# Optimization experiments

Measured on AMD Instinct MI355X. Metric: run time of the kernel, lower is better.

Reference implementation:

```python
import jax, jax.numpy as jnp
import numpy as np


def _extract_patches_same(x, k):
    # x: [B, h, w, C] -> patches [B, h, w, C, k*k] (channel-major, patch-minor,
    # matching the depthwise-conv based extract_patches_xla layout that the
    # reshape (group, C//group, k^2) in CarafeConvolution assumes).
    b, h, w, c = x.shape
    pad = k // 2
    xp = jnp.pad(x, ((0, 0), (pad, pad), (pad, pad), (0, 0)))
    shifts = [xp[:, di:di + h, dj:dj + w, :] for di in range(k) for dj in range(k)]
    return jnp.stack(shifts, axis=-1)  # [B, h, w, C, k^2]


def _nearest_idx(out_size, in_size):
    # tf.image.resize nearest with half-pixel centers
    scale = in_size / out_size
    idx = jnp.floor((jnp.arange(out_size) + 0.5) * scale).astype(jnp.int32)
    return jnp.clip(idx, 0, in_size - 1)


def setup_inputs() -> dict:
    key = jax.random.key(0)
    k1, k2 = jax.random.split(key)
    features = jax.random.normal(k1, (2, 64, 64, 256), dtype=jnp.float32)
    masks = jax.random.uniform(k2, (2, 128, 128, 25), dtype=jnp.float32)
    return {"features": features, "masks": masks, "kernel_size": 5}


def reference(features, masks, kernel_size):
    k = kernel_size
    B, H, W, C1 = masks.shape
    _, h, w, C0 = features.shape
    group = C1 // (k * k)
    # im2col patch extraction at low resolution
    patches = _extract_patches_same(features, k)  # [B, h, w, C0, k^2]
    # nearest-neighbor upsample patches to mask resolution
    ih = _nearest_idx(H, h)
    iw = _nearest_idx(W, w)
    patches = patches[:, ih][:, :, iw]  # [B, H, W, C0, k^2]
    # grouped adaptive-kernel reassembly
    feats = patches.reshape(B, H, W, group, C0 // group, k * k)
    m = masks.reshape(B, H, W, group, k * k)
    out = jnp.einsum('bhwgcp,bhwgp->bhwgc', feats, m)
    return out.reshape(B, H, W, C0)
```

## Files before the change

kernel.cpp:

```cpp
#include <hip/hip_runtime.h>


#define C0   256
#define HLO  64
#define WLO  64
#define HHI  128
#define WHI  128
#define K    5
#define KK   25

__global__ __launch_bounds__(256) void carafe_quad_kernel(
    const float* __restrict__ feat,
    const float* __restrict__ mask,
    float* __restrict__ out)
{
    const int wid = __builtin_amdgcn_readfirstlane(
        blockIdx.x * 4 + (threadIdx.x >> 6));
    const int lane = threadIdx.x & 63;
    const int c    = lane * 4;

    const int b  = wid >> 12;
    const int y0 = (wid >> 6) & 63;
    const int x0 = wid & 63;

    const int Y0 = y0 * 2;
    const int X0 = x0 * 2;

    const float* fbase = feat + ((size_t)b * HLO * WLO) * C0;
    const float* mbase = mask + ((size_t)((b * HHI + Y0) * WHI + X0)) * KK;
    const float* m00 = mbase;
    const float* m01 = mbase + KK;
    const float* m10 = mbase + WHI * KK;
    const float* m11 = mbase + WHI * KK + KK;

    float4 a00 = make_float4(0.f, 0.f, 0.f, 0.f);
    float4 a01 = make_float4(0.f, 0.f, 0.f, 0.f);
    float4 a10 = make_float4(0.f, 0.f, 0.f, 0.f);
    float4 a11 = make_float4(0.f, 0.f, 0.f, 0.f);

    #pragma unroll
    for (int di = 0; di < K; ++di) {
        const int   y  = y0 + di - 2;
        const int   yc = min(max(y, 0), HLO - 1);
        const float vy = ((unsigned)y < (unsigned)HLO) ? 1.f : 0.f;
        #pragma unroll
        for (int dj = 0; dj < K; ++dj) {
            const int   x  = x0 + dj - 2;
            const int   xc = min(max(x, 0), WLO - 1);
            const float v  = ((unsigned)x < (unsigned)WLO) ? vy : 0.f;

            float4 f = *(const float4*)(fbase + (size_t)(yc * WLO + xc) * C0 + c);
            f.x *= v; f.y *= v; f.z *= v; f.w *= v;

            const int p = di * K + dj;
            const float w00 = m00[p];
            const float w01 = m01[p];
            const float w10 = m10[p];
            const float w11 = m11[p];
            a00.x = fmaf(f.x, w00, a00.x); a00.y = fmaf(f.y, w00, a00.y);
            a00.z = fmaf(f.z, w00, a00.z); a00.w = fmaf(f.w, w00, a00.w);
            a01.x = fmaf(f.x, w01, a01.x); a01.y = fmaf(f.y, w01, a01.y);
            a01.z = fmaf(f.z, w01, a01.z); a01.w = fmaf(f.w, w01, a01.w);
            a10.x = fmaf(f.x, w10, a10.x); a10.y = fmaf(f.y, w10, a10.y);
            a10.z = fmaf(f.z, w10, a10.z); a10.w = fmaf(f.w, w10, a10.w);
            a11.x = fmaf(f.x, w11, a11.x); a11.y = fmaf(f.y, w11, a11.y);
            a11.z = fmaf(f.z, w11, a11.z); a11.w = fmaf(f.w, w11, a11.w);
        }
    }

    float* obase = out + ((size_t)((b * HHI + Y0) * WHI + X0)) * C0 + c;
    *(float4*)(obase)                 = a00;
    *(float4*)(obase + C0)            = a01;
    *(float4*)(obase + WHI * C0)      = a10;
    *(float4*)(obase + WHI * C0 + C0) = a11;
}

extern "C" void kernel_launch(void* const* d_in, const int* in_sizes, int n_in,
                              void* d_out, int out_size, void* d_ws, size_t ws_size,
                              hipStream_t stream) {
    const float* feat = (const float*)d_in[0];
    const float* mask = (const float*)d_in[1];
    float* out = (float*)d_out;

    carafe_quad_kernel<<<8192 / 4, 256, 0, stream>>>(feat, mask, out);
}
```

Measured before the change: 79.89 us.

## Process two adjacent low-res columns per wave and remap blocks per XCD

Each wave now computes a 2x4 block of high-res outputs from two neighbouring low-res pixels. It walks a shared 6-wide window of feature columns, so one load feeds both pixels' 5x5 taps: 30 feature loads per row set instead of 50. Block indices are also remapped so that each XCD handles a contiguous range of (batch, row) pairs, which is meant to improve L2 locality of the feature reads. The cost is twice as many accumulators per thread and half as many waves, which lowers occupancy and latency hiding.

```diff
diff --git a/kernel.cpp b/kernel.cpp
--- a/kernel.cpp
+++ b/kernel.cpp
@@ -9,34 +9,36 @@
 #define K    5
 #define KK   25
 
-__global__ __launch_bounds__(256) void carafe_quad_kernel(
+__global__ __launch_bounds__(256) void carafe_kernel(
     const float* __restrict__ feat,
     const float* __restrict__ mask,
     float* __restrict__ out)
 {
-    const int wid = __builtin_amdgcn_readfirstlane(
-        blockIdx.x * 4 + (threadIdx.x >> 6));
+    const int wv   = __builtin_amdgcn_readfirstlane(threadIdx.x >> 6);
+    const int bid  = blockIdx.x;
+    const int xcd  = bid & 7;
+    const int i    = bid >> 3;
+    const int r    = xcd * 16 + (i & 15);
+    const int xblk = i >> 4;
+    const int b    = r >> 6;
+    const int y0   = r & 63;
+    const int x0   = xblk * 8 + wv * 2;
     const int lane = threadIdx.x & 63;
     const int c    = lane * 4;
-
-    const int b  = wid >> 12;
-    const int y0 = (wid >> 6) & 63;
-    const int x0 = wid & 63;
 
     const int Y0 = y0 * 2;
     const int X0 = x0 * 2;
 
-    const float* fbase = feat + ((size_t)b * HLO * WLO) * C0;
-    const float* mbase = mask + ((size_t)((b * HHI + Y0) * WHI + X0)) * KK;
-    const float* m00 = mbase;
-    const float* m01 = mbase + KK;
-    const float* m10 = mbase + WHI * KK;
-    const float* m11 = mbase + WHI * KK + KK;
+    const float* fbase = feat + (size_t)b * HLO * WLO * C0;
+    const float* mrow0 = mask + (size_t)((b * HHI + Y0) * WHI + X0) * KK;
+    const float* mrow1 = mrow0 + WHI * KK;
 
-    float4 a00 = make_float4(0.f, 0.f, 0.f, 0.f);
-    float4 a01 = make_float4(0.f, 0.f, 0.f, 0.f);
-    float4 a10 = make_float4(0.f, 0.f, 0.f, 0.f);
-    float4 a11 = make_float4(0.f, 0.f, 0.f, 0.f);
+    float4 acc[2][4];
+    #pragma unroll
+    for (int rr = 0; rr < 2; ++rr)
+        #pragma unroll
+        for (int qq = 0; qq < 4; ++qq)
+            acc[rr][qq] = make_float4(0.f, 0.f, 0.f, 0.f);
 
     #pragma unroll
     for (int di = 0; di < K; ++di) {
@@ -44,35 +46,53 @@
         const int   yc = min(max(y, 0), HLO - 1);
         const float vy = ((unsigned)y < (unsigned)HLO) ? 1.f : 0.f;
         #pragma unroll
-        for (int dj = 0; dj < K; ++dj) {
-            const int   x  = x0 + dj - 2;
+        for (int t = 0; t < 6; ++t) {
+            const int   x  = x0 + t - 2;
             const int   xc = min(max(x, 0), WLO - 1);
             const float v  = ((unsigned)x < (unsigned)WLO) ? vy : 0.f;
 
             float4 f = *(const float4*)(fbase + (size_t)(yc * WLO + xc) * C0 + c);
             f.x *= v; f.y *= v; f.z *= v; f.w *= v;
 
-            const int p = di * K + dj;
-            const float w00 = m00[p];
-            const float w01 = m01[p];
-            const float w10 = m10[p];
-            const float w11 = m11[p];
-            a00.x = fmaf(f.x, w00, a00.x); a00.y = fmaf(f.y, w00, a00.y);
-            a00.z = fmaf(f.z, w00, a00.z); a00.w = fmaf(f.w, w00, a00.w);
-            a01.x = fmaf(f.x, w01, a01.x); a01.y = fmaf(f.y, w01, a01.y);
-            a01.z = fmaf(f.z, w01, a01.z); a01.w = fmaf(f.w, w01, a01.w);
-            a10.x = fmaf(f.x, w10, a10.x); a10.y = fmaf(f.y, w10, a10.y);
-            a10.z = fmaf(f.z, w10, a10.z); a10.w = fmaf(f.w, w10, a10.w);
-            a11.x = fmaf(f.x, w11, a11.x); a11.y = fmaf(f.y, w11, a11.y);
-            a11.z = fmaf(f.z, w11, a11.z); a11.w = fmaf(f.w, w11, a11.w);
+            if (t <= 4) {
+                const int p = di * K + t;
+                #pragma unroll
+                for (int rr = 0; rr < 2; ++rr) {
+                    const float* mr = rr ? mrow1 : mrow0;
+                    #pragma unroll
+                    for (int qq = 0; qq < 2; ++qq) {
+                        const float wgt = mr[qq * KK + p];
+                        acc[rr][qq].x = fmaf(f.x, wgt, acc[rr][qq].x);
+                        acc[rr][qq].y = fmaf(f.y, wgt, acc[rr][qq].y);
+                        acc[rr][qq].z = fmaf(f.z, wgt, acc[rr][qq].z);
+                        acc[rr][qq].w = fmaf(f.w, wgt, acc[rr][qq].w);
+                    }
+                }
+            }
+            if (t >= 1) {
+                const int p = di * K + t - 1;
+                #pragma unroll
+                for (int rr = 0; rr < 2; ++rr) {
+                    const float* mr = rr ? mrow1 : mrow0;
+                    #pragma unroll
+                    for (int qq = 2; qq < 4; ++qq) {
+                        const float wgt = mr[qq * KK + p];
+                        acc[rr][qq].x = fmaf(f.x, wgt, acc[rr][qq].x);
+                        acc[rr][qq].y = fmaf(f.y, wgt, acc[rr][qq].y);
+                        acc[rr][qq].z = fmaf(f.z, wgt, acc[rr][qq].z);
+                        acc[rr][qq].w = fmaf(f.w, wgt, acc[rr][qq].w);
+                    }
+                }
+            }
         }
     }
 
-    float* obase = out + ((size_t)((b * HHI + Y0) * WHI + X0)) * C0 + c;
-    *(float4*)(obase)                 = a00;
-    *(float4*)(obase + C0)            = a01;
-    *(float4*)(obase + WHI * C0)      = a10;
-    *(float4*)(obase + WHI * C0 + C0) = a11;
+    float* ob = out + (size_t)((b * HHI + Y0) * WHI + X0) * C0 + c;
+    #pragma unroll
+    for (int rr = 0; rr < 2; ++rr)
+        #pragma unroll
+        for (int qq = 0; qq < 4; ++qq)
+            *(float4*)(ob + (size_t)(rr * WHI + qq) * C0) = acc[rr][qq];
 }
 
 extern "C" void kernel_launch(void* const* d_in, const int* in_sizes, int n_in,
@@ -82,5 +102,5 @@
     const float* mask = (const float*)d_in[1];
     float* out = (float*)d_out;
 
-    carafe_quad_kernel<<<8192 / 4, 256, 0, stream>>>(feat, mask, out);
+    carafe_kernel<<<1024, 256, 0, stream>>>(feat, mask, out);
 }
```

Measured after the change: 79.61 us. No clear change (-0.4%).
